# Kernel tuning notes

Measured on AMD Instinct MI355X. Metric: run time of the kernel, lower is better.

The kernel has to match this reference:

```python
import jax, jax.numpy as jnp
import numpy as np

N = 50000
E = 800000
IN_C, HID, OUT_C = 128, 128, 64
EPS = 1e-5


def gcn_conv(x, edge_index, W, b):
    # x: [N, F_in], edge_index: [2, E], W: [F_in, F_out], b: [F_out]
    src, dst = edge_index[0], edge_index[1]
    h = x @ W  # [N, F_out]
    # degree with self-loops (edge weight 1)
    deg = 1.0 + jax.ops.segment_sum(jnp.ones((E,), h.dtype), dst, num_segments=N)
    dinv = jax.lax.rsqrt(deg)  # deg^{-1/2}
    coef = dinv[src] * dinv[dst]  # [E]
    msg = h[src] * coef[:, None]  # gather + scale
    agg = jax.ops.segment_sum(msg, dst, num_segments=N)
    agg = agg + h * (dinv * dinv)[:, None]  # self-loop term deg^{-1}
    return agg + b


def bn_eval(x, gamma, beta, mean, var):
    return (x - mean) * jax.lax.rsqrt(var + EPS) * gamma + beta


def leaky(x):
    return jnp.where(x > 0, x, 0.1 * x)


def setup_inputs() -> dict:
    key = jax.random.key(0)
    ks = jax.random.split(key, 12)
    x = jax.random.normal(ks[0], (N, IN_C), jnp.float32)
    edge_index = jax.random.randint(ks[1], (2, E), 0, N, dtype=jnp.int64)
    s1 = 1.0 / np.sqrt(IN_C)
    s2 = 1.0 / np.sqrt(HID)
    W1 = jax.random.uniform(ks[2], (IN_C, HID), jnp.float32, -s1, s1)
    b1 = jnp.zeros((HID,), jnp.float32)
    W2 = jax.random.uniform(ks[3], (HID, HID), jnp.float32, -s2, s2)
    b2 = jnp.zeros((HID,), jnp.float32)
    W3 = jax.random.uniform(ks[4], (HID, OUT_C), jnp.float32, -s2, s2)
    b3 = jnp.zeros((OUT_C,), jnp.float32)
    g1 = jnp.ones((HID,), jnp.float32)
    be1 = jnp.zeros((HID,), jnp.float32)
    m1 = 0.1 * jax.random.normal(ks[5], (HID,), jnp.float32)
    v1 = jax.random.uniform(ks[6], (HID,), jnp.float32, 0.5, 1.5)
    g2 = jnp.ones((HID,), jnp.float32)
    be2 = jnp.zeros((HID,), jnp.float32)
    m2 = 0.1 * jax.random.normal(ks[7], (HID,), jnp.float32)
    v2 = jax.random.uniform(ks[8], (HID,), jnp.float32, 0.5, 1.5)
    return dict(x=x, edge_index=edge_index, W1=W1, b1=b1, g1=g1, be1=be1, m1=m1, v1=v1,
                W2=W2, b2=b2, g2=g2, be2=be2, m2=m2, v2=v2, W3=W3, b3=b3)


def reference(x, edge_index, W1, b1, g1, be1, m1, v1, W2, b2, g2, be2, m2, v2, W3, b3):
    h = gcn_conv(x, edge_index, W1, b1)
    h = leaky(bn_eval(h, g1, be1, m1, v1))
    # dropout is identity at inference
    h = gcn_conv(h, edge_index, W2, b2)
    h = leaky(bn_eval(h, g2, be2, m2, v2))
    z = gcn_conv(h, edge_index, W3, b3)
    return z
```

## Files before the change

### kernel.cpp

```cpp
#include <hip/hip_runtime.h>
#include <hip/hip_fp16.h>


#define LRELU_SLOPE 0.1f
#define BN_EPS 1e-5f
#define BCAP 20480

typedef _Float16 half8 __attribute__((ext_vector_type(8)));
typedef float f32x4 __attribute__((ext_vector_type(4)));

__global__ void init_bcur(int* __restrict__ bcur) {
    int i = threadIdx.x;
    if (i < 64) bcur[i] = i * BCAP;
}

__global__ __launch_bounds__(256) void bin_pass(const int* __restrict__ src,
                                                const int* __restrict__ dst, int E,
                                                int* __restrict__ bcur,
                                                unsigned long long* __restrict__ pairs) {
    __shared__ int sd[3200], ss[3200];
    __shared__ int lcur[64];
    const int tid = threadIdx.x;
    const int chunk = (E + gridDim.x - 1) / gridDim.x;
    const int e0 = blockIdx.x * chunk;
    const int ecnt = min(chunk, E - e0);
    for (int j = tid; j < ecnt; j += 256) {
        sd[j] = dst[e0 + j];
        ss[j] = src[e0 + j];
    }
    if (tid < 64) lcur[tid] = 0;
    __syncthreads();
    for (int j = tid; j < ecnt; j += 256) atomicAdd(&lcur[sd[j] >> 10], 1);
    __syncthreads();
    if (tid < 64) lcur[tid] = atomicAdd(&bcur[tid], lcur[tid]);
    __syncthreads();
    for (int j = tid; j < ecnt; j += 256) {
        const int b = sd[j] >> 10;
        const int pos = atomicAdd(&lcur[b], 1);
        pairs[pos] = ((unsigned long long)(unsigned)ss[j] << 32) | (unsigned)sd[j];
    }
}

__global__ __launch_bounds__(512) void hist_bucket(const unsigned long long* __restrict__ pairs,
                                                   const int* __restrict__ bcur,
                                                   int* __restrict__ cnt, int N) {
    __shared__ int h[1024];
    const int b = blockIdx.x;
    const int base = b << 10;
    const int nn = min(1024, N - base);
    const int cntb = bcur[b] - b * BCAP;
    for (int i = threadIdx.x; i < 1024; i += 512) h[i] = 0;
    __syncthreads();
    const unsigned long long* pb = pairs + (size_t)b * BCAP;
    for (int j = threadIdx.x; j < cntb; j += 512) {
        const int d = (int)(pb[j] & 0xffffffffull);
        atomicAdd(&h[d - base], 1);
    }
    __syncthreads();
    for (int i = threadIdx.x; i < nn; i += 512) cnt[base + i] = h[i];
}

__global__ void scan1(const int* __restrict__ cnt, int* __restrict__ incl,
                      int* __restrict__ part, int n) {
    __shared__ int s[256];
    int tid = threadIdx.x;
    int gid = blockIdx.x * 256 + tid;
    int v = (gid < n) ? cnt[gid] : 0;
    s[tid] = v;
    __syncthreads();
    for (int off = 1; off < 256; off <<= 1) {
        int t = (tid >= off) ? s[tid - off] : 0;
        __syncthreads();
        s[tid] += t;
        __syncthreads();
    }
    if (gid < n) incl[gid] = s[tid];
    if (tid == 255) part[blockIdx.x] = s[255];
}

__global__ void scan2(const int* __restrict__ part, int* __restrict__ poff, int nb) {
    __shared__ int s[256];
    int tid = threadIdx.x;
    int v = (tid < nb) ? part[tid] : 0;
    s[tid] = v;
    __syncthreads();
    for (int off = 1; off < 256; off <<= 1) {
        int t = (tid >= off) ? s[tid - off] : 0;
        __syncthreads();
        s[tid] += t;
        __syncthreads();
    }
    poff[tid] = s[tid] - v;
}

__global__ void scan3(const int* __restrict__ cnt, const int* __restrict__ incl,
                      const int* __restrict__ poff, int* __restrict__ row_ptr,
                      float* __restrict__ dinv, int n, int E) {
    int gid = blockIdx.x * 256 + threadIdx.x;
    if (gid < n) {
        int c = cnt[gid];
        row_ptr[gid] = incl[gid] - c + poff[blockIdx.x];
        dinv[gid] = rsqrtf(1.0f + (float)c);
    }
    if (gid == 0) row_ptr[n] = E;
}

__global__ __launch_bounds__(512) void build_csr(const unsigned long long* __restrict__ pairs,
                                                 const int* __restrict__ bcur,
                                                 const int* __restrict__ row_ptr,
                                                 int* __restrict__ ssrc_g, int N) {
    __shared__ int cur[1024];
    const int b = blockIdx.x;
    const int base = b << 10;
    const int nn = min(1024, N - base);
    const int cntb = bcur[b] - b * BCAP;
    for (int i = threadIdx.x; i < nn; i += 512) cur[i] = row_ptr[base + i];
    __syncthreads();
    const unsigned long long* pb = pairs + (size_t)b * BCAP;
    for (int j = threadIdx.x; j < cntb; j += 512) {
        const unsigned long long p = pb[j];
        const int d = (int)(p & 0xffffffffull);
        const int s = (int)(p >> 32);
        const int pos = atomicAdd(&cur[d - base], 1);
        ssrc_g[pos] = s;
    }
}

__global__ void prep_w(const float* __restrict__ W1, const float* __restrict__ W2,
                       const float* __restrict__ W3, _Float16* __restrict__ W1t,
                       _Float16* __restrict__ W2t, _Float16* __restrict__ W3t) {
    int i = blockIdx.x * 256 + threadIdx.x;
    if (i < 16384) {
        int k = i >> 7, c = i & 127;
        W1t[c * 136 + k] = (_Float16)W1[i];
    } else if (i < 32768) {
        int j = i - 16384;
        int k = j >> 7, c = j & 127;
        W2t[c * 136 + k] = (_Float16)W2[j];
    } else if (i < 40960) {
        int j = i - 32768;
        int k = j >> 6, c = j & 63;
        W3t[c * 136 + k] = (_Float16)W3[j];
    }
}

template <int NC, bool AF32>
__global__ __launch_bounds__(256) void gemm_mfma(const void* __restrict__ Ain,
                                                 const _Float16* __restrict__ Wt,
                                                 const float* __restrict__ dinv,
                                                 __half* __restrict__ H, int nrows) {
    constexpr int NT = NC / 16;
    constexpr int SPH = (NC == 128) ? 136 : 88;
    __shared__ _Float16 smem[NC * 136];

    const int tid = threadIdx.x;
    const int row0 = blockIdx.x * 64;

    {
        const uint4* src = reinterpret_cast<const uint4*>(Wt);
        uint4* dst = reinterpret_cast<uint4*>(smem);
        for (int i = tid; i < NC * 17; i += 256) dst[i] = src[i];
    }
    __syncthreads();

    const int w = tid >> 6;
    const int lane = tid & 63;
    const int l15 = lane & 15;
    const int kg = lane >> 4;

    int ar = row0 + w * 16 + l15;
    if (ar > nrows - 1) ar = nrows - 1;
    half8 a[4];
#pragma unroll
    for (int ks = 0; ks < 4; ++ks) {
        const int cb = ks * 32 + kg * 8;
        if constexpr (AF32) {
            const float* Xf = (const float*)Ain;
            const float4 x0 = *reinterpret_cast<const float4*>(&Xf[(size_t)ar * 128 + cb]);
            const float4 x1 = *reinterpret_cast<const float4*>(&Xf[(size_t)ar * 128 + cb + 4]);
            half8 av;
            av[0] = (_Float16)x0.x; av[1] = (_Float16)x0.y;
            av[2] = (_Float16)x0.z; av[3] = (_Float16)x0.w;
            av[4] = (_Float16)x1.x; av[5] = (_Float16)x1.y;
            av[6] = (_Float16)x1.z; av[7] = (_Float16)x1.w;
            a[ks] = av;
        } else {
            const __half* Xh = (const __half*)Ain;
            a[ks] = *reinterpret_cast<const half8*>(&Xh[(size_t)ar * 128 + cb]);
        }
    }

    f32x4 acc[NT];
#pragma unroll
    for (int nt = 0; nt < NT; ++nt) acc[nt] = {0.f, 0.f, 0.f, 0.f};

#pragma unroll
    for (int nt = 0; nt < NT; ++nt) {
        const int c = nt * 16 + l15;
#pragma unroll
        for (int ks = 0; ks < 4; ++ks) {
            const half8 b = *reinterpret_cast<const half8*>(&smem[c * 136 + ks * 32 + kg * 8]);
            acc[nt] = __builtin_amdgcn_mfma_f32_16x16x32_f16(a[ks], b, acc[nt], 0, 0, 0);
        }
    }

    __syncthreads();

    float dv[4];
#pragma unroll
    for (int r = 0; r < 4; ++r) {
        int gr = row0 + w * 16 + kg * 4 + r;
        if (gr > nrows - 1) gr = nrows - 1;
        dv[r] = dinv[gr];
    }
    _Float16* Hl = smem;
#pragma unroll
    for (int nt = 0; nt < NT; ++nt) {
#pragma unroll
        for (int r = 0; r < 4; ++r) {
            Hl[(w * 16 + kg * 4 + r) * SPH + nt * 16 + l15] = (_Float16)(acc[nt][r] * dv[r]);
        }
    }
    __syncthreads();

    constexpr int CG = NC / 8;
    for (int i = tid; i < 64 * CG; i += 256) {
        const int row = i / CG, cg = i % CG;
        const int gr = row0 + row;
        if (gr < nrows) {
            *reinterpret_cast<uint4*>(&H[(size_t)gr * NC + cg * 8]) =
                *reinterpret_cast<const uint4*>(&Hl[row * SPH + cg * 8]);
        }
    }
}

__device__ __forceinline__ float2 u2f2(unsigned u) {
    __half2 h;
    *reinterpret_cast<unsigned*>(&h) = u;
    return __half22float2(h);
}

template <int NC, bool BN, bool HOUT>
__global__ __launch_bounds__(256) void agg_h(
    const __half* __restrict__ H, const int* __restrict__ row_ptr,
    const int* __restrict__ ssrc, const float* __restrict__ dinv,
    const float* __restrict__ b, const float* __restrict__ g,
    const float* __restrict__ be, const float* __restrict__ m,
    const float* __restrict__ v, void* __restrict__ out, int n) {
    constexpr int FPT = NC / 32;
    const int tid = threadIdx.x;
    const int node = blockIdx.x * 8 + (tid >> 5);
    const int lane = tid & 31;
    const int f0 = lane * FPT;
    if (node >= n) return;

    const int e0 = row_ptr[node];
    const int e1 = row_ptr[node + 1];

    if constexpr (FPT == 4) {
        uint2 su = *reinterpret_cast<const uint2*>(&H[(size_t)node * NC + f0]);
        float2 slo = u2f2(su.x), shi = u2f2(su.y);
        float4 A0 = {slo.x, slo.y, shi.x, shi.y};
        float4 A1 = {0, 0, 0, 0}, A2 = {0, 0, 0, 0}, A3 = {0, 0, 0, 0};
        int e = e0;
        for (; e + 3 < e1; e += 4) {
            const int sA = ssrc[e], sB = ssrc[e + 1], sC = ssrc[e + 2], sD = ssrc[e + 3];
            const uint2 uA = *reinterpret_cast<const uint2*>(&H[(size_t)sA * NC + f0]);
            const uint2 uB = *reinterpret_cast<const uint2*>(&H[(size_t)sB * NC + f0]);
            const uint2 uC = *reinterpret_cast<const uint2*>(&H[(size_t)sC * NC + f0]);
            const uint2 uD = *reinterpret_cast<const uint2*>(&H[(size_t)sD * NC + f0]);
            float2 l, h;
            l = u2f2(uA.x); h = u2f2(uA.y);
            A0.x += l.x; A0.y += l.y; A0.z += h.x; A0.w += h.y;
            l = u2f2(uB.x); h = u2f2(uB.y);
            A1.x += l.x; A1.y += l.y; A1.z += h.x; A1.w += h.y;
            l = u2f2(uC.x); h = u2f2(uC.y);
            A2.x += l.x; A2.y += l.y; A2.z += h.x; A2.w += h.y;
            l = u2f2(uD.x); h = u2f2(uD.y);
            A3.x += l.x; A3.y += l.y; A3.z += h.x; A3.w += h.y;
        }
        for (; e < e1; ++e) {
            const uint2 u = *reinterpret_cast<const uint2*>(&H[(size_t)ssrc[e] * NC + f0]);
            float2 l = u2f2(u.x), h = u2f2(u.y);
            A1.x += l.x; A1.y += l.y; A1.z += h.x; A1.w += h.y;
        }
        float4 acc;
        acc.x = (A0.x + A1.x) + (A2.x + A3.x);
        acc.y = (A0.y + A1.y) + (A2.y + A3.y);
        acc.z = (A0.z + A1.z) + (A2.z + A3.z);
        acc.w = (A0.w + A1.w) + (A2.w + A3.w);
        const float dn = dinv[node];
        float o[4] = {acc.x * dn + b[f0], acc.y * dn + b[f0 + 1],
                      acc.z * dn + b[f0 + 2], acc.w * dn + b[f0 + 3]};
        if constexpr (BN) {
#pragma unroll
            for (int j = 0; j < 4; ++j) {
                float val = (o[j] - m[f0 + j]) * rsqrtf(v[f0 + j] + BN_EPS) * g[f0 + j] + be[f0 + j];
                o[j] = val > 0.f ? val : LRELU_SLOPE * val;
            }
        }
        if constexpr (HOUT) {
            __half2 p0 = __floats2half2_rn(o[0], o[1]);
            __half2 p1 = __floats2half2_rn(o[2], o[3]);
            uint2 st;
            st.x = *reinterpret_cast<unsigned*>(&p0);
            st.y = *reinterpret_cast<unsigned*>(&p1);
            *reinterpret_cast<uint2*>(&((__half*)out)[(size_t)node * NC + f0]) = st;
        } else {
            float4 ov = {o[0], o[1], o[2], o[3]};
            *reinterpret_cast<float4*>(&((float*)out)[(size_t)node * NC + f0]) = ov;
        }
    } else {
        unsigned su = *reinterpret_cast<const unsigned*>(&H[(size_t)node * NC + f0]);
        float2 A0 = u2f2(su);
        float2 A1 = {0, 0}, A2 = {0, 0}, A3 = {0, 0};
        int e = e0;
        for (; e + 3 < e1; e += 4) {
            const int sA = ssrc[e], sB = ssrc[e + 1], sC = ssrc[e + 2], sD = ssrc[e + 3];
            const unsigned uA = *reinterpret_cast<const unsigned*>(&H[(size_t)sA * NC + f0]);
            const unsigned uB = *reinterpret_cast<const unsigned*>(&H[(size_t)sB * NC + f0]);
            const unsigned uC = *reinterpret_cast<const unsigned*>(&H[(size_t)sC * NC + f0]);
            const unsigned uD = *reinterpret_cast<const unsigned*>(&H[(size_t)sD * NC + f0]);
            float2 f;
            f = u2f2(uA); A0.x += f.x; A0.y += f.y;
            f = u2f2(uB); A1.x += f.x; A1.y += f.y;
            f = u2f2(uC); A2.x += f.x; A2.y += f.y;
            f = u2f2(uD); A3.x += f.x; A3.y += f.y;
        }
        for (; e < e1; ++e) {
            float2 f = u2f2(*reinterpret_cast<const unsigned*>(&H[(size_t)ssrc[e] * NC + f0]));
            A1.x += f.x; A1.y += f.y;
        }
        float2 acc;
        acc.x = (A0.x + A1.x) + (A2.x + A3.x);
        acc.y = (A0.y + A1.y) + (A2.y + A3.y);
        const float dn = dinv[node];
        float o0 = acc.x * dn + b[f0];
        float o1 = acc.y * dn + b[f0 + 1];
        if constexpr (BN) {
            o0 = (o0 - m[f0]) * rsqrtf(v[f0] + BN_EPS) * g[f0] + be[f0];
            o0 = o0 > 0.f ? o0 : LRELU_SLOPE * o0;
            o1 = (o1 - m[f0 + 1]) * rsqrtf(v[f0 + 1] + BN_EPS) * g[f0 + 1] + be[f0 + 1];
            o1 = o1 > 0.f ? o1 : LRELU_SLOPE * o1;
        }
        if constexpr (HOUT) {
            __half2 p0 = __floats2half2_rn(o0, o1);
            *reinterpret_cast<unsigned*>(&((__half*)out)[(size_t)node * NC + f0]) =
                *reinterpret_cast<unsigned*>(&p0);
        } else {
            float2 ov = {o0, o1};
            *reinterpret_cast<float2*>(&((float*)out)[(size_t)node * NC + f0]) = ov;
        }
    }
}

extern "C" void kernel_launch(void* const* d_in, const int* in_sizes, int n_in,
                              void* d_out, int out_size, void* d_ws, size_t ws_size,
                              hipStream_t stream) {
    const float* x  = (const float*)d_in[0];
    const int* ei   = (const int*)d_in[1];
    const float* W1 = (const float*)d_in[2];
    const float* b1 = (const float*)d_in[3];
    const float* g1 = (const float*)d_in[4];
    const float* be1= (const float*)d_in[5];
    const float* m1 = (const float*)d_in[6];
    const float* v1 = (const float*)d_in[7];
    const float* W2 = (const float*)d_in[8];
    const float* b2 = (const float*)d_in[9];
    const float* g2 = (const float*)d_in[10];
    const float* be2= (const float*)d_in[11];
    const float* m2 = (const float*)d_in[12];
    const float* v2 = (const float*)d_in[13];
    const float* W3 = (const float*)d_in[14];
    const float* b3 = (const float*)d_in[15];
    float* out = (float*)d_out;

    const int N = in_sizes[0] / 128;
    const int E = in_sizes[1] / 2;
    const int* srcIdx = ei;
    const int* dstIdx = ei + E;
    const int nbuck = (N + 1023) >> 10;

    char* p = (char*)d_ws;
    auto carve = [&](size_t bytes) -> void* {
        void* r = (void*)p;
        p += (bytes + 255) & ~(size_t)255;
        return r;
    };
    int* cnt       = (int*)carve((size_t)N * 4);
    int* incl      = (int*)carve((size_t)N * 4);
    int* part      = (int*)carve(1024);
    int* poff      = (int*)carve(1024);
    int* row_ptr   = (int*)carve((size_t)(N + 1) * 4);
    int* bcur      = (int*)carve(64 * 4);
    float* dinv    = (float*)carve((size_t)N * 4);
    int* ssrc      = (int*)carve((size_t)E * 4);
    unsigned long long* pairs = (unsigned long long*)carve((size_t)nbuck * BCAP * 8);
    __half* Hb     = (__half*)carve((size_t)N * 128 * 2);
    __half* Xb     = (__half*)carve((size_t)N * 128 * 2);
    _Float16* W1t  = (_Float16*)carve(128 * 136 * 2);
    _Float16* W2t  = (_Float16*)carve(128 * 136 * 2);
    _Float16* W3t  = (_Float16*)carve(64 * 136 * 2);
    (void)ws_size; (void)n_in; (void)out_size;

    const int nb_n = (N + 255) / 256;

    prep_w<<<160, 256, 0, stream>>>(W1, W2, W3, W1t, W2t, W3t);
    init_bcur<<<1, 64, 0, stream>>>(bcur);
    bin_pass<<<256, 256, 0, stream>>>(srcIdx, dstIdx, E, bcur, pairs);
    hist_bucket<<<nbuck, 512, 0, stream>>>(pairs, bcur, cnt, N);
    scan1<<<nb_n, 256, 0, stream>>>(cnt, incl, part, N);
    scan2<<<1, 256, 0, stream>>>(part, poff, nb_n);
    scan3<<<nb_n, 256, 0, stream>>>(cnt, incl, poff, row_ptr, dinv, N, E);
    build_csr<<<nbuck, 512, 0, stream>>>(pairs, bcur, row_ptr, ssrc, N);

    const int gb = (N + 63) / 64;
    const int ab = (N + 7) / 8;

    gemm_mfma<128, true><<<gb, 256, 0, stream>>>(x, W1t, dinv, Hb, N);
    agg_h<128, true, true><<<ab, 256, 0, stream>>>(
        Hb, row_ptr, ssrc, dinv, b1, g1, be1, m1, v1, Xb, N);

    gemm_mfma<128, false><<<gb, 256, 0, stream>>>(Xb, W2t, dinv, Hb, N);
    agg_h<128, true, true><<<ab, 256, 0, stream>>>(
        Hb, row_ptr, ssrc, dinv, b2, g2, be2, m2, v2, Xb, N);

    gemm_mfma<64, false><<<gb, 256, 0, stream>>>(Xb, W3t, dinv, Hb, N);
    agg_h<64, false, false><<<ab, 256, 0, stream>>>(
        Hb, row_ptr, ssrc, dinv, b3, nullptr, nullptr, nullptr, nullptr, out, N);
}
```

Baseline: 266.1 us.

## Fold bias and batchnorm into scale/shift, merge setup kernels, unroll gather by eight

Precomputes per-feature scale and shift that combine bias and eval batchnorm, so the aggregation epilogue does one FMA instead of reloading five parameter arrays and calling rsqrt per element. It merges the weight prep with bcur init, merges scan2 and scan3 into one kernel that reduces the partial sums per block, and doubles bin_pass blocks with smaller shared buffers. The aggregation inner loop now issues eight independent gathers per iteration for more memory-level parallelism, at the cost of more registers.

```diff
diff --git a/kernel.cpp b/kernel.cpp
--- a/kernel.cpp
+++ b/kernel.cpp
@@ -9,126 +9,20 @@
 typedef _Float16 half8 __attribute__((ext_vector_type(8)));
 typedef float f32x4 __attribute__((ext_vector_type(4)));
 
-__global__ void init_bcur(int* __restrict__ bcur) {
-    int i = threadIdx.x;
-    if (i < 64) bcur[i] = i * BCAP;
-}
-
-__global__ __launch_bounds__(256) void bin_pass(const int* __restrict__ src,
-                                                const int* __restrict__ dst, int E,
-                                                int* __restrict__ bcur,
-                                                unsigned long long* __restrict__ pairs) {
-    __shared__ int sd[3200], ss[3200];
-    __shared__ int lcur[64];
-    const int tid = threadIdx.x;
-    const int chunk = (E + gridDim.x - 1) / gridDim.x;
-    const int e0 = blockIdx.x * chunk;
-    const int ecnt = min(chunk, E - e0);
-    for (int j = tid; j < ecnt; j += 256) {
-        sd[j] = dst[e0 + j];
-        ss[j] = src[e0 + j];
-    }
-    if (tid < 64) lcur[tid] = 0;
-    __syncthreads();
-    for (int j = tid; j < ecnt; j += 256) atomicAdd(&lcur[sd[j] >> 10], 1);
-    __syncthreads();
-    if (tid < 64) lcur[tid] = atomicAdd(&bcur[tid], lcur[tid]);
-    __syncthreads();
-    for (int j = tid; j < ecnt; j += 256) {
-        const int b = sd[j] >> 10;
-        const int pos = atomicAdd(&lcur[b], 1);
-        pairs[pos] = ((unsigned long long)(unsigned)ss[j] << 32) | (unsigned)sd[j];
-    }
-}
-
-__global__ __launch_bounds__(512) void hist_bucket(const unsigned long long* __restrict__ pairs,
-                                                   const int* __restrict__ bcur,
-                                                   int* __restrict__ cnt, int N) {
-    __shared__ int h[1024];
-    const int b = blockIdx.x;
-    const int base = b << 10;
-    const int nn = min(1024, N - base);
-    const int cntb = bcur[b] - b * BCAP;
-    for (int i = threadIdx.x; i < 1024; i += 512) h[i] = 0;
-    __syncthreads();
-    const unsigned long long* pb = pairs + (size_t)b * BCAP;
-    for (int j = threadIdx.x; j < cntb; j += 512) {
-        const int d = (int)(pb[j] & 0xffffffffull);
-        atomicAdd(&h[d - base], 1);
-    }
-    __syncthreads();
-    for (int i = threadIdx.x; i < nn; i += 512) cnt[base + i] = h[i];
-}
-
-__global__ void scan1(const int* __restrict__ cnt, int* __restrict__ incl,
-                      int* __restrict__ part, int n) {
-    __shared__ int s[256];
-    int tid = threadIdx.x;
-    int gid = blockIdx.x * 256 + tid;
-    int v = (gid < n) ? cnt[gid] : 0;
-    s[tid] = v;
-    __syncthreads();
-    for (int off = 1; off < 256; off <<= 1) {
-        int t = (tid >= off) ? s[tid - off] : 0;
-        __syncthreads();
-        s[tid] += t;
-        __syncthreads();
-    }
-    if (gid < n) incl[gid] = s[tid];
-    if (tid == 255) part[blockIdx.x] = s[255];
-}
-
-__global__ void scan2(const int* __restrict__ part, int* __restrict__ poff, int nb) {
-    __shared__ int s[256];
-    int tid = threadIdx.x;
-    int v = (tid < nb) ? part[tid] : 0;
-    s[tid] = v;
-    __syncthreads();
-    for (int off = 1; off < 256; off <<= 1) {
-        int t = (tid >= off) ? s[tid - off] : 0;
-        __syncthreads();
-        s[tid] += t;
-        __syncthreads();
-    }
-    poff[tid] = s[tid] - v;
-}
-
-__global__ void scan3(const int* __restrict__ cnt, const int* __restrict__ incl,
-                      const int* __restrict__ poff, int* __restrict__ row_ptr,
-                      float* __restrict__ dinv, int n, int E) {
-    int gid = blockIdx.x * 256 + threadIdx.x;
-    if (gid < n) {
-        int c = cnt[gid];
-        row_ptr[gid] = incl[gid] - c + poff[blockIdx.x];
-        dinv[gid] = rsqrtf(1.0f + (float)c);
-    }
-    if (gid == 0) row_ptr[n] = E;
-}
-
-__global__ __launch_bounds__(512) void build_csr(const unsigned long long* __restrict__ pairs,
-                                                 const int* __restrict__ bcur,
-                                                 const int* __restrict__ row_ptr,
-                                                 int* __restrict__ ssrc_g, int N) {
-    __shared__ int cur[1024];
-    const int b = blockIdx.x;
-    const int base = b << 10;
-    const int nn = min(1024, N - base);
-    const int cntb = bcur[b] - b * BCAP;
-    for (int i = threadIdx.x; i < nn; i += 512) cur[i] = row_ptr[base + i];
-    __syncthreads();
-    const unsigned long long* pb = pairs + (size_t)b * BCAP;
-    for (int j = threadIdx.x; j < cntb; j += 512) {
-        const unsigned long long p = pb[j];
-        const int d = (int)(p & 0xffffffffull);
-        const int s = (int)(p >> 32);
-        const int pos = atomicAdd(&cur[d - base], 1);
-        ssrc_g[pos] = s;
-    }
-}
-
-__global__ void prep_w(const float* __restrict__ W1, const float* __restrict__ W2,
-                       const float* __restrict__ W3, _Float16* __restrict__ W1t,
-                       _Float16* __restrict__ W2t, _Float16* __restrict__ W3t) {
+__global__ void prep_all(const float* __restrict__ W1, const float* __restrict__ W2,
+                         const float* __restrict__ W3, _Float16* __restrict__ W1t,
+                         _Float16* __restrict__ W2t, _Float16* __restrict__ W3t,
+                         const float* __restrict__ b1, const float* __restrict__ g1,
+                         const float* __restrict__ be1, const float* __restrict__ m1,
+                         const float* __restrict__ v1,
+                         const float* __restrict__ b2, const float* __restrict__ g2,
+                         const float* __restrict__ be2, const float* __restrict__ m2,
+                         const float* __restrict__ v2,
+                         const float* __restrict__ b3,
+                         float* __restrict__ sc1, float* __restrict__ sh1,
+                         float* __restrict__ sc2, float* __restrict__ sh2,
+                         float* __restrict__ sc3, float* __restrict__ sh3,
+                         int* __restrict__ bcur) {
     int i = blockIdx.x * 256 + threadIdx.x;
     if (i < 16384) {
         int k = i >> 7, c = i & 127;
@@ -141,6 +35,130 @@
         int j = i - 32768;
         int k = j >> 6, c = j & 63;
         W3t[c * 136 + k] = (_Float16)W3[j];
+    } else if (i < 41088) {
+        int f = i - 40960;
+        float s = g1[f] * rsqrtf(v1[f] + BN_EPS);
+        sc1[f] = s;
+        sh1[f] = (b1[f] - m1[f]) * s + be1[f];
+    } else if (i < 41216) {
+        int f = i - 41088;
+        float s = g2[f] * rsqrtf(v2[f] + BN_EPS);
+        sc2[f] = s;
+        sh2[f] = (b2[f] - m2[f]) * s + be2[f];
+    } else if (i < 41280) {
+        int f = i - 41216;
+        sc3[f] = 1.0f;
+        sh3[f] = b3[f];
+    } else if (i < 41344) {
+        bcur[i - 41280] = (i - 41280) * BCAP;
+    }
+}
+
+__global__ __launch_bounds__(256) void bin_pass(const int* __restrict__ src,
+                                                const int* __restrict__ dst, int E,
+                                                int* __restrict__ bcur,
+                                                unsigned long long* __restrict__ pairs) {
+    __shared__ int sd[1664], ss[1664];
+    __shared__ int lcur[64];
+    const int tid = threadIdx.x;
+    const int chunk = (E + gridDim.x - 1) / gridDim.x;
+    const int e0 = blockIdx.x * chunk;
+    const int ecnt = min(chunk, E - e0);
+    for (int j = tid; j < ecnt; j += 256) {
+        sd[j] = dst[e0 + j];
+        ss[j] = src[e0 + j];
+    }
+    if (tid < 64) lcur[tid] = 0;
+    __syncthreads();
+    for (int j = tid; j < ecnt; j += 256) atomicAdd(&lcur[sd[j] >> 10], 1);
+    __syncthreads();
+    if (tid < 64) lcur[tid] = atomicAdd(&bcur[tid], lcur[tid]);
+    __syncthreads();
+    for (int j = tid; j < ecnt; j += 256) {
+        const int b = sd[j] >> 10;
+        const int pos = atomicAdd(&lcur[b], 1);
+        pairs[pos] = ((unsigned long long)(unsigned)ss[j] << 32) | (unsigned)sd[j];
+    }
+}
+
+__global__ __launch_bounds__(512) void hist_bucket(const unsigned long long* __restrict__ pairs,
+                                                   const int* __restrict__ bcur,
+                                                   int* __restrict__ cnt, int N) {
+    __shared__ int h[1024];
+    const int b = blockIdx.x;
+    const int base = b << 10;
+    const int nn = min(1024, N - base);
+    const int cntb = bcur[b] - b * BCAP;
+    for (int i = threadIdx.x; i < 1024; i += 512) h[i] = 0;
+    __syncthreads();
+    const unsigned long long* pb = pairs + (size_t)b * BCAP;
+    for (int j = threadIdx.x; j < cntb; j += 512) {
+        const int d = (int)(pb[j] & 0xffffffffull);
+        atomicAdd(&h[d - base], 1);
+    }
+    __syncthreads();
+    for (int i = threadIdx.x; i < nn; i += 512) cnt[base + i] = h[i];
+}
+
+__global__ void scan1(const int* __restrict__ cnt, int* __restrict__ incl,
+                      int* __restrict__ part, int n) {
+    __shared__ int s[256];
+    int tid = threadIdx.x;
+    int gid = blockIdx.x * 256 + tid;
+    int v = (gid < n) ? cnt[gid] : 0;
+    s[tid] = v;
+    __syncthreads();
+    for (int off = 1; off < 256; off <<= 1) {
+        int t = (tid >= off) ? s[tid - off] : 0;
+        __syncthreads();
+        s[tid] += t;
+        __syncthreads();
+    }
+    if (gid < n) incl[gid] = s[tid];
+    if (tid == 255) part[blockIdx.x] = s[255];
+}
+
+__global__ void scan23(const int* __restrict__ cnt, const int* __restrict__ incl,
+                       const int* __restrict__ part, int* __restrict__ row_ptr,
+                       float* __restrict__ dinv, int n, int E) {
+    __shared__ int red[256];
+    const int tid = threadIdx.x;
+    int acc = 0;
+    for (int i = tid; i < blockIdx.x; i += 256) acc += part[i];
+    red[tid] = acc;
+    __syncthreads();
+    for (int off = 128; off > 0; off >>= 1) {
+        if (tid < off) red[tid] += red[tid + off];
+        __syncthreads();
+    }
+    const int pof = red[0];
+    const int gid = blockIdx.x * 256 + tid;
+    if (gid < n) {
+        int c = cnt[gid];
+        row_ptr[gid] = incl[gid] - c + pof;
+        dinv[gid] = rsqrtf(1.0f + (float)c);
+    }
+    if (gid == 0) row_ptr[n] = E;
+}
+
+__global__ __launch_bounds__(512) void build_csr(const unsigned long long* __restrict__ pairs,
+                                                 const int* __restrict__ bcur,
+                                                 const int* __restrict__ row_ptr,
+                                                 int* __restrict__ ssrc_g, int N) {
+    __shared__ int cur[1024];
+    const int b = blockIdx.x;
+    const int base = b << 10;
+    const int nn = min(1024, N - base);
+    const int cntb = bcur[b] - b * BCAP;
+    for (int i = threadIdx.x; i < nn; i += 512) cur[i] = row_ptr[base + i];
+    __syncthreads();
+    const unsigned long long* pb = pairs + (size_t)b * BCAP;
+    for (int j = threadIdx.x; j < cntb; j += 512) {
+        const unsigned long long p = pb[j];
+        const int d = (int)(p & 0xffffffffull);
+        const int s = (int)(p >> 32);
+        const int pos = atomicAdd(&cur[d - base], 1);
+        ssrc_g[pos] = s;
     }
 }
 
@@ -240,13 +258,12 @@
     return __half22float2(h);
 }
 
-template <int NC, bool BN, bool HOUT>
+template <int NC, bool ACT, bool HOUT>
 __global__ __launch_bounds__(256) void agg_h(
     const __half* __restrict__ H, const int* __restrict__ row_ptr,
     const int* __restrict__ ssrc, const float* __restrict__ dinv,
-    const float* __restrict__ b, const float* __restrict__ g,
-    const float* __restrict__ be, const float* __restrict__ m,
-    const float* __restrict__ v, void* __restrict__ out, int n) {
+    const float* __restrict__ sc, const float* __restrict__ sh,
+    void* __restrict__ out, int n) {
     constexpr int FPT = NC / 32;
     const int tid = threadIdx.x;
     const int node = blockIdx.x * 8 + (tid >> 5);
@@ -263,21 +280,20 @@
         float4 A0 = {slo.x, slo.y, shi.x, shi.y};
         float4 A1 = {0, 0, 0, 0}, A2 = {0, 0, 0, 0}, A3 = {0, 0, 0, 0};
         int e = e0;
-        for (; e + 3 < e1; e += 4) {
-            const int sA = ssrc[e], sB = ssrc[e + 1], sC = ssrc[e + 2], sD = ssrc[e + 3];
-            const uint2 uA = *reinterpret_cast<const uint2*>(&H[(size_t)sA * NC + f0]);
-            const uint2 uB = *reinterpret_cast<const uint2*>(&H[(size_t)sB * NC + f0]);
-            const uint2 uC = *reinterpret_cast<const uint2*>(&H[(size_t)sC * NC + f0]);
-            const uint2 uD = *reinterpret_cast<const uint2*>(&H[(size_t)sD * NC + f0]);
-            float2 l, h;
-            l = u2f2(uA.x); h = u2f2(uA.y);
-            A0.x += l.x; A0.y += l.y; A0.z += h.x; A0.w += h.y;
-            l = u2f2(uB.x); h = u2f2(uB.y);
-            A1.x += l.x; A1.y += l.y; A1.z += h.x; A1.w += h.y;
-            l = u2f2(uC.x); h = u2f2(uC.y);
-            A2.x += l.x; A2.y += l.y; A2.z += h.x; A2.w += h.y;
-            l = u2f2(uD.x); h = u2f2(uD.y);
-            A3.x += l.x; A3.y += l.y; A3.z += h.x; A3.w += h.y;
+        for (; e + 7 < e1; e += 8) {
+            int s[8];
+#pragma unroll
+            for (int j = 0; j < 8; ++j) s[j] = ssrc[e + j];
+            uint2 u[8];
+#pragma unroll
+            for (int j = 0; j < 8; ++j)
+                u[j] = *reinterpret_cast<const uint2*>(&H[(size_t)s[j] * NC + f0]);
+#pragma unroll
+            for (int j = 0; j < 8; ++j) {
+                float2 l = u2f2(u[j].x), h = u2f2(u[j].y);
+                float4& A = (j & 3) == 0 ? A0 : (j & 3) == 1 ? A1 : (j & 3) == 2 ? A2 : A3;
+                A.x += l.x; A.y += l.y; A.z += h.x; A.w += h.y;
+            }
         }
         for (; e < e1; ++e) {
             const uint2 u = *reinterpret_cast<const uint2*>(&H[(size_t)ssrc[e] * NC + f0]);
@@ -290,14 +306,16 @@
         acc.z = (A0.z + A1.z) + (A2.z + A3.z);
         acc.w = (A0.w + A1.w) + (A2.w + A3.w);
         const float dn = dinv[node];
-        float o[4] = {acc.x * dn + b[f0], acc.y * dn + b[f0 + 1],
-                      acc.z * dn + b[f0 + 2], acc.w * dn + b[f0 + 3]};
-        if constexpr (BN) {
-#pragma unroll
-            for (int j = 0; j < 4; ++j) {
-                float val = (o[j] - m[f0 + j]) * rsqrtf(v[f0 + j] + BN_EPS) * g[f0 + j] + be[f0 + j];
-                o[j] = val > 0.f ? val : LRELU_SLOPE * val;
-            }
+        const float4 scv = *reinterpret_cast<const float4*>(&sc[f0]);
+        const float4 shv = *reinterpret_cast<const float4*>(&sh[f0]);
+        float o[4];
+        o[0] = fmaf(acc.x * dn, scv.x, shv.x);
+        o[1] = fmaf(acc.y * dn, scv.y, shv.y);
+        o[2] = fmaf(acc.z * dn, scv.z, shv.z);
+        o[3] = fmaf(acc.w * dn, scv.w, shv.w);
+        if constexpr (ACT) {
+#pragma unroll
+            for (int j = 0; j < 4; ++j) o[j] = o[j] > 0.f ? o[j] : LRELU_SLOPE * o[j];
         }
         if constexpr (HOUT) {
             __half2 p0 = __floats2half2_rn(o[0], o[1]);
@@ -315,17 +333,20 @@
         float2 A0 = u2f2(su);
         float2 A1 = {0, 0}, A2 = {0, 0}, A3 = {0, 0};
         int e = e0;
-        for (; e + 3 < e1; e += 4) {
-            const int sA = ssrc[e], sB = ssrc[e + 1], sC = ssrc[e + 2], sD = ssrc[e + 3];
-            const unsigned uA = *reinterpret_cast<const unsigned*>(&H[(size_t)sA * NC + f0]);
-            const unsigned uB = *reinterpret_cast<const unsigned*>(&H[(size_t)sB * NC + f0]);
-            const unsigned uC = *reinterpret_cast<const unsigned*>(&H[(size_t)sC * NC + f0]);
-            const unsigned uD = *reinterpret_cast<const unsigned*>(&H[(size_t)sD * NC + f0]);
-            float2 f;
-            f = u2f2(uA); A0.x += f.x; A0.y += f.y;
-            f = u2f2(uB); A1.x += f.x; A1.y += f.y;
-            f = u2f2(uC); A2.x += f.x; A2.y += f.y;
-            f = u2f2(uD); A3.x += f.x; A3.y += f.y;
+        for (; e + 7 < e1; e += 8) {
+            int s[8];
+#pragma unroll
+            for (int j = 0; j < 8; ++j) s[j] = ssrc[e + j];
+            unsigned u[8];
+#pragma unroll
+            for (int j = 0; j < 8; ++j)
+                u[j] = *reinterpret_cast<const unsigned*>(&H[(size_t)s[j] * NC + f0]);
+#pragma unroll
+            for (int j = 0; j < 8; ++j) {
+                float2 f = u2f2(u[j]);
+                float2& A = (j & 3) == 0 ? A0 : (j & 3) == 1 ? A1 : (j & 3) == 2 ? A2 : A3;
+                A.x += f.x; A.y += f.y;
+            }
         }
         for (; e < e1; ++e) {
             float2 f = u2f2(*reinterpret_cast<const unsigned*>(&H[(size_t)ssrc[e] * NC + f0]));
@@ -335,12 +356,12 @@
         acc.x = (A0.x + A1.x) + (A2.x + A3.x);
         acc.y = (A0.y + A1.y) + (A2.y + A3.y);
         const float dn = dinv[node];
-        float o0 = acc.x * dn + b[f0];
-        float o1 = acc.y * dn + b[f0 + 1];
-        if constexpr (BN) {
-            o0 = (o0 - m[f0]) * rsqrtf(v[f0] + BN_EPS) * g[f0] + be[f0];
+        const float2 scv = *reinterpret_cast<const float2*>(&sc[f0]);
+        const float2 shv = *reinterpret_cast<const float2*>(&sh[f0]);
+        float o0 = fmaf(acc.x * dn, scv.x, shv.x);
+        float o1 = fmaf(acc.y * dn, scv.y, shv.y);
+        if constexpr (ACT) {
             o0 = o0 > 0.f ? o0 : LRELU_SLOPE * o0;
-            o1 = (o1 - m[f0 + 1]) * rsqrtf(v[f0 + 1] + BN_EPS) * g[f0 + 1] + be[f0 + 1];
             o1 = o1 > 0.f ? o1 : LRELU_SLOPE * o1;
         }
         if constexpr (HOUT) {
@@ -390,7 +411,6 @@
     int* cnt       = (int*)carve((size_t)N * 4);
     int* incl      = (int*)carve((size_t)N * 4);
     int* part      = (int*)carve(1024);
-    int* poff      = (int*)carve(1024);
     int* row_ptr   = (int*)carve((size_t)(N + 1) * 4);
     int* bcur      = (int*)carve(64 * 4);
     float* dinv    = (float*)carve((size_t)N * 4);
@@ -401,17 +421,23 @@
     _Float16* W1t  = (_Float16*)carve(128 * 136 * 2);
     _Float16* W2t  = (_Float16*)carve(128 * 136 * 2);
     _Float16* W3t  = (_Float16*)carve(64 * 136 * 2);
+    float* sc1     = (float*)carve(128 * 4);
+    float* sh1     = (float*)carve(128 * 4);
+    float* sc2     = (float*)carve(128 * 4);
+    float* sh2     = (float*)carve(128 * 4);
+    float* sc3     = (float*)carve(64 * 4);
+    float* sh3     = (float*)carve(64 * 4);
     (void)ws_size; (void)n_in; (void)out_size;
 
     const int nb_n = (N + 255) / 256;
 
-    prep_w<<<160, 256, 0, stream>>>(W1, W2, W3, W1t, W2t, W3t);
-    init_bcur<<<1, 64, 0, stream>>>(bcur);
-    bin_pass<<<256, 256, 0, stream>>>(srcIdx, dstIdx, E, bcur, pairs);
+    prep_all<<<162, 256, 0, stream>>>(W1, W2, W3, W1t, W2t, W3t,
+                                      b1, g1, be1, m1, v1, b2, g2, be2, m2, v2, b3,
+                                      sc1, sh1, sc2, sh2, sc3, sh3, bcur);
+    bin_pass<<<512, 256, 0, stream>>>(srcIdx, dstIdx, E, bcur, pairs);
     hist_bucket<<<nbuck, 512, 0, stream>>>(pairs, bcur, cnt, N);
     scan1<<<nb_n, 256, 0, stream>>>(cnt, incl, part, N);
-    scan2<<<1, 256, 0, stream>>>(part, poff, nb_n);
-    scan3<<<nb_n, 256, 0, stream>>>(cnt, incl, poff, row_ptr, dinv, N, E);
+    scan23<<<nb_n, 256, 0, stream>>>(cnt, incl, part, row_ptr, dinv, N, E);
     build_csr<<<nbuck, 512, 0, stream>>>(pairs, bcur, row_ptr, ssrc, N);
 
     const int gb = (N + 63) / 64;
@@ -419,13 +445,13 @@
 
     gemm_mfma<128, true><<<gb, 256, 0, stream>>>(x, W1t, dinv, Hb, N);
     agg_h<128, true, true><<<ab, 256, 0, stream>>>(
-        Hb, row_ptr, ssrc, dinv, b1, g1, be1, m1, v1, Xb, N);
+        Hb, row_ptr, ssrc, dinv, sc1, sh1, Xb, N);
 
     gemm_mfma<128, false><<<gb, 256, 0, stream>>>(Xb, W2t, dinv, Hb, N);
     agg_h<128, true, true><<<ab, 256, 0, stream>>>(
-        Hb, row_ptr, ssrc, dinv, b2, g2, be2, m2, v2, Xb, N);
+        Hb, row_ptr, ssrc, dinv, sc2, sh2, Xb, N);
 
     gemm_mfma<64, false><<<gb, 256, 0, stream>>>(Xb, W3t, dinv, Hb, N);
     agg_h<64, false, false><<<ab, 256, 0, stream>>>(
-        Hb, row_ptr, ssrc, dinv, b3, nullptr, nullptr, nullptr, nullptr, out, N);
-}
+        Hb, row_ptr, ssrc, dinv, sc3, sh3, out, N);
+}
```

Result: no change. 269.7 us (+1.3%).
